# Kernel optimization log

Measured on AMD Instinct MI355X. Metric: run time of the kernel, lower is better.

The kernel has to match this reference:

```python
import jax, jax.numpy as jnp
import numpy as np

B, S, H, NH, HD = 2, 2048, 4096, 32, 128  # batch, seq, hidden, heads, head_dim
THETA = 10000.0
SCALE = HD ** -0.5


def setup_inputs() -> dict:
    key = jax.random.key(0)
    k1, k2, k3 = jax.random.split(key, 3)
    hidden_states = jax.random.normal(k1, (B, S, H), jnp.float32) * 0.02
    w_pack = jax.random.normal(k2, (3 * H, H), jnp.float32) * 0.02  # fused QKV weight
    w_o = jax.random.normal(k3, (H, H), jnp.float32) * 0.02
    positions = jnp.broadcast_to(jnp.arange(S, dtype=jnp.int32), (B, S))
    return {"positions": positions, "hidden_states": hidden_states,
            "w_pack": w_pack, "w_o": w_o}


def _apply_rope(x, positions):
    # x: [B, S, NH, HD]; neox-style (rotate-half) RoPE over full head_dim
    inv_freq = 1.0 / (THETA ** (jnp.arange(0, HD, 2, dtype=jnp.float32) / HD))  # [HD/2]
    ang = positions.astype(jnp.float32)[..., None] * inv_freq  # [B, S, HD/2]
    cos = jnp.cos(ang)[:, :, None, :]  # [B, S, 1, HD/2]
    sin = jnp.sin(ang)[:, :, None, :]
    x1, x2 = x[..., : HD // 2], x[..., HD // 2 :]
    return jnp.concatenate([x1 * cos - x2 * sin, x2 * cos + x1 * sin], axis=-1)


def reference(positions, hidden_states, w_pack, w_o):
    # Fused QKV projection then split (W_pack, bias-free)
    qkv = jnp.einsum('bsh,oh->bso', hidden_states, w_pack)  # [B, S, 3H]
    q, k, v = jnp.split(qkv, 3, axis=-1)
    q = q.reshape(B, S, NH, HD)
    k = k.reshape(B, S, NH, HD)
    v = v.reshape(B, S, NH, HD)
    q = _apply_rope(q, positions)
    k = _apply_rope(k, positions)
    # Causal scaled-dot-product attention
    scores = jnp.einsum('bqhd,bkhd->bhqk', q, k) * SCALE
    causal = jnp.tril(jnp.ones((S, S), dtype=bool))
    scores = jnp.where(causal, scores, jnp.float32(-1e9))
    probs = jax.nn.softmax(scores, axis=-1)
    attn = jnp.einsum('bhqk,bkhd->bqhd', probs, v).reshape(B, S, H)
    return jnp.einsum('bsh,oh->bso', attn, w_o)  # o_proj, bias-free
```

## Files before the change

### kernel.cpp

```cpp
#include <hip/hip_runtime.h>

typedef short short8 __attribute__((ext_vector_type(8)));
typedef float f32x4 __attribute__((ext_vector_type(4)));
typedef unsigned short u16;

static constexpr int BATCH = 2, S = 2048, H = 4096, NHEAD = 32, HDIM = 128;

__device__ __forceinline__ u16 f2b(float f) {
  union { float f; unsigned u; } v; v.f = f;
  return (u16)((v.u + 0x7fffu + ((v.u >> 16) & 1u)) >> 16);
}
__device__ __forceinline__ float b2f(u16 h) {
  union { unsigned u; float f; } v; v.u = ((unsigned)h) << 16;
  return v.f;
}

__device__ __forceinline__ void gl16(const u16* g, u16* l) {
  __builtin_amdgcn_global_load_lds((__attribute__((address_space(1))) void*)g,
                                   (__attribute__((address_space(3))) void*)l,
                                   16, 0, 0);
}

#define MFMA(acc, a, b) \
  acc = __builtin_amdgcn_mfma_f32_16x16x32_bf16(a, b, acc, 0, 0, 0)

__global__ __launch_bounds__(256) void cvt_bf16(const float* __restrict__ in,
                                                u16* __restrict__ out) {
  size_t i = ((size_t)blockIdx.x * 256 + threadIdx.x) * 4;
  float4 v = *(const float4*)(in + i);
  ushort4 o = { f2b(v.x), f2b(v.y), f2b(v.z), f2b(v.w) };
  *(ushort4*)(out + i) = o;
}

__global__ __launch_bounds__(256) void rope_table(float* __restrict__ tab) {
  int idx = blockIdx.x * 256 + threadIdx.x;
  int p = idx >> 6, f = idx & 63;
  float freq = __powf(10000.0f, -(float)f * (1.0f / 64.0f));
  float a = (float)p * freq;
  tab[(size_t)p * 128 + f] = cosf(a);
  tab[(size_t)p * 128 + 64 + f] = sinf(a);
}

template <int MODE>
__global__ __launch_bounds__(512, 2) void gemm256(
    const u16* __restrict__ A, const u16* __restrict__ B, void* __restrict__ C,
    int M, int N, int K, const int* __restrict__ pos,
    const float* __restrict__ tab, u16* __restrict__ qr, u16* __restrict__ kr,
    u16* __restrict__ vt) {
  __shared__ u16 SMEM[69632];
  u16* AL = SMEM;
  u16* BL = SMEM + 32768;
  const int nbn = N >> 8;
  const int nwg = (M >> 8) * nbn;
  const int bid = blockIdx.x;
  const int wg = (bid & 7) * (nwg >> 3) + (bid >> 3);
  const int bm = wg / nbn, bn = wg % nbn;
  const int tid = threadIdx.x, lane = tid & 63;
  const int w = tid >> 6, wm = w >> 2, wn = w & 3;
  const int hi = lane >> 4, lo = lane & 15;
  const int nk = K >> 6;

  const u16* Abase = A + (size_t)(bm * 256) * K;
  const u16* Bbase = B + (size_t)(bn * 256) * K;

#define STG_A(buf, half, kt)                                                   \
  { _Pragma("unroll") for (int i = 0; i < 2; ++i) {                            \
      int c = tid + i * 512, r = c >> 3, s = c & 7;                            \
      gl16(Abase + (size_t)((half) * 128 + r) * K + (kt) * 64 +                \
               ((s ^ (r & 7)) * 8),                                            \
           &AL[((buf) * 2 + (half)) * 8192 + c * 8]);                          \
    } }
#define STG_B(buf, half, kt)                                                   \
  { _Pragma("unroll") for (int i = 0; i < 2; ++i) {                            \
      int c = tid + i * 512, r = c >> 3, s = c & 7;                            \
      gl16(Bbase + (size_t)((half) * 128 + r) * K + (kt) * 64 +                \
               ((s ^ (r & 7)) * 8),                                            \
           &BL[((buf) * 2 + (half)) * 8192 + c * 8]);                          \
    } }
#define BARTOP()                                                               \
  do { __builtin_amdgcn_s_barrier();                                           \
       __builtin_amdgcn_sched_barrier(0); } while (0)

  f32x4 acc[8][4] = {};

  STG_A(0, 0, 0) STG_A(0, 1, 0) STG_B(0, 0, 0) STG_B(0, 1, 0)
  if (nk > 1) {
    STG_B(1, 0, 1) STG_B(1, 1, 1)
    asm volatile("s_waitcnt vmcnt(4)" ::: "memory");
  } else {
    asm volatile("s_waitcnt vmcnt(0)" ::: "memory");
  }
  __builtin_amdgcn_sched_barrier(0);

  short8 af[4][2], bfA[2][2], bfB[2][2];

  for (int t = 0; t < nk; ++t) {
    const int cur = t & 1;
    const u16* Awave = AL + (cur * 2 + wm) * 8192;
    const u16* Bwave = BL + (cur * 2 + (wn >> 1)) * 8192;
    const int lrB = (wn & 1) * 64;

    BARTOP();
    if (t + 1 < nk) STG_A(cur ^ 1, 0, t + 1)
#pragma unroll
    for (int mi = 0; mi < 4; ++mi)
#pragma unroll
      for (int ks = 0; ks < 2; ++ks)
        af[mi][ks] = *(const short8*)&Awave[(mi * 16 + lo) * 64 +
                                            (((ks * 4 + hi) ^ (lo & 7)) * 8)];
#pragma unroll
    for (int ni = 0; ni < 2; ++ni)
#pragma unroll
      for (int ks = 0; ks < 2; ++ks)
        bfA[ni][ks] = *(const short8*)&Bwave[(lrB + ni * 16 + lo) * 64 +
                                             (((ks * 4 + hi) ^ (lo & 7)) * 8)];

    BARTOP();
    if (t + 1 < nk) STG_A(cur ^ 1, 1, t + 1)
#pragma unroll
    for (int ni = 0; ni < 2; ++ni)
#pragma unroll
      for (int ks = 0; ks < 2; ++ks)
        bfB[ni][ks] = *(const short8*)&Bwave[(lrB + 32 + ni * 16 + lo) * 64 +
                                             (((ks * 4 + hi) ^ (lo & 7)) * 8)];
    __builtin_amdgcn_s_setprio(1);
#pragma unroll
    for (int mi = 0; mi < 4; ++mi)
#pragma unroll
      for (int ni = 0; ni < 2; ++ni)
#pragma unroll
        for (int ks = 0; ks < 2; ++ks)
          MFMA(acc[mi][ni], af[mi][ks], bfA[ni][ks]);
    __builtin_amdgcn_s_setprio(0);

    BARTOP();
    if (t + 2 < nk) STG_B(cur, 0, t + 2)
    __builtin_amdgcn_s_setprio(1);
#pragma unroll
    for (int mi = 0; mi < 4; ++mi)
#pragma unroll
      for (int ni = 0; ni < 2; ++ni)
#pragma unroll
        for (int ks = 0; ks < 2; ++ks)
          MFMA(acc[mi][2 + ni], af[mi][ks], bfB[ni][ks]);
    __builtin_amdgcn_s_setprio(0);
#pragma unroll
    for (int mi = 0; mi < 4; ++mi)
#pragma unroll
      for (int ks = 0; ks < 2; ++ks)
        af[mi][ks] = *(const short8*)&Awave[((64 + mi * 16 + lo)) * 64 +
                                            (((ks * 4 + hi) ^ (lo & 7)) * 8)];

    BARTOP();
    if (t + 2 < nk) STG_B(cur, 1, t + 2)
    __builtin_amdgcn_s_setprio(1);
#pragma unroll
    for (int mi = 0; mi < 4; ++mi)
#pragma unroll
      for (int ni = 0; ni < 2; ++ni)
#pragma unroll
        for (int ks = 0; ks < 2; ++ks)
          MFMA(acc[4 + mi][2 + ni], af[mi][ks], bfB[ni][ks]);
#pragma unroll
    for (int mi = 0; mi < 4; ++mi)
#pragma unroll
      for (int ni = 0; ni < 2; ++ni)
#pragma unroll
        for (int ks = 0; ks < 2; ++ks)
          MFMA(acc[4 + mi][ni], af[mi][ks], bfA[ni][ks]);
    __builtin_amdgcn_s_setprio(0);
    if (t + 2 < nk) {
      asm volatile("s_waitcnt vmcnt(4)" ::: "memory");
    } else {
      asm volatile("s_waitcnt vmcnt(0)" ::: "memory");
    }
    __builtin_amdgcn_sched_barrier(0);
  }

  if constexpr (MODE == 1) {
#pragma unroll
    for (int mf = 0; mf < 8; ++mf)
#pragma unroll
      for (int nf = 0; nf < 4; ++nf)
#pragma unroll
        for (int j = 0; j < 4; ++j) {
          size_t idx = (size_t)(bm * 256 + wm * 128 + mf * 16 + hi * 4 + j) * N +
                       bn * 256 + wn * 64 + nf * 16 + lo;
          ((float*)C)[idx] = acc[mf][nf][j];
        }
  } else {
    const int SP = 272;
    u16* E = SMEM;
    __syncthreads();
#pragma unroll
    for (int mf = 0; mf < 8; ++mf)
#pragma unroll
      for (int nf = 0; nf < 4; ++nf)
#pragma unroll
        for (int j = 0; j < 4; ++j)
          E[(wm * 128 + mf * 16 + hi * 4 + j) * SP + wn * 64 + nf * 16 + lo] =
              f2b(acc[mf][nf][j]);
    __syncthreads();

    const int grow0 = bm * 256, gcol0 = bn * 256;
    const int bb = grow0 >> 11, s0 = grow0 & 2047;
    if (gcol0 < 8192) {
      for (int task = tid; task < 8192; task += 512) {
        int row = task >> 5, g = task & 31;
        int gcol = gcol0 + g * 8;
        int d = gcol & 127, f0 = d & 63;
        int p = pos[grow0 + row];
        const float* cp = tab + (size_t)p * 128 + f0;
        float4 ca = *(const float4*)cp, cb = *(const float4*)(cp + 4);
        float4 sa = *(const float4*)(cp + 64), sb = *(const float4*)(cp + 68);
        float cv[8] = {ca.x, ca.y, ca.z, ca.w, cb.x, cb.y, cb.z, cb.w};
        float sv[8] = {sa.x, sa.y, sa.z, sa.w, sb.x, sb.y, sb.z, sb.w};
        short8 x = *(const short8*)&E[row * SP + g * 8];
        short8 xo = *(const short8*)&E[row * SP + (g ^ 8) * 8];
        float sgn = (d < 64) ? -1.0f : 1.0f;
        unsigned word[4];
#pragma unroll
        for (int pr = 0; pr < 4; ++pr) {
          float v0 = b2f((u16)x[2 * pr]) * cv[2 * pr] +
                     sgn * b2f((u16)xo[2 * pr]) * sv[2 * pr];
          float v1 = b2f((u16)x[2 * pr + 1]) * cv[2 * pr + 1] +
                     sgn * b2f((u16)xo[2 * pr + 1]) * sv[2 * pr + 1];
          word[pr] = (unsigned)f2b(v0) | ((unsigned)f2b(v1) << 16);
        }
        int hidx = gcol >> 7;
        u16* outp = (hidx < 32) ? qr : kr;
        int nh = (hidx < 32) ? hidx : hidx - 32;
        size_t dst = ((size_t)(bb * 32 + nh) * 2048 + (s0 + row)) * 128 + d;
        uint4 o = {word[0], word[1], word[2], word[3]};
        *(uint4*)&outp[dst] = o;
      }
    } else {
      for (int task = tid; task < 8192; task += 512) {
        int kbl = task >> 11;
        int hh = (task >> 10) & 1;
        int c = task & 1023;
        int f = c >> 6, l = c & 63;
        int ks2 = f >> 3, db = f & 7, hi2 = l >> 4, lo2 = l & 15;
        int base = (kbl * 64 + ks2 * 32 + hi2 * 8) * SP + hh * 128 + db * 16 + lo2;
        unsigned e0 = E[base], e1 = E[base + SP], e2 = E[base + 2 * SP],
                 e3 = E[base + 3 * SP], e4 = E[base + 4 * SP],
                 e5 = E[base + 5 * SP], e6 = E[base + 6 * SP],
                 e7 = E[base + 7 * SP];
        int nh = ((gcol0 - 8192) >> 7) + hh;
        size_t dst = ((size_t)(bb * 32 + nh) * 2048 + (s0 + kbl * 64)) * 128 +
                     (size_t)c * 8;
        uint4 o = {e0 | (e1 << 16), e2 | (e3 << 16), e4 | (e5 << 16),
                   e6 | (e7 << 16)};
        *(uint4*)&vt[dst] = o;
      }
    }
  }
}

__global__ __launch_bounds__(256, 2) void flash_fwd(const u16* __restrict__ q,
                                                    const u16* __restrict__ k,
                                                    const u16* __restrict__ vt,
                                                    u16* __restrict__ o) {
  __shared__ u16 KB[2][64 * 128];
  __shared__ u16 VB[2][64 * 128];
  __shared__ u16 Ps[4][16 * 64];
  const int nqt = S / 64;
  const int qt = (nqt - 1) - ((int)blockIdx.x % nqt);
  const int bh = blockIdx.x / nqt;
  const int tid = threadIdx.x, lane = tid & 63, w = tid >> 6;
  const int hi = lane >> 4, lo = lane & 15;

  const u16* qg = q + ((size_t)bh * S + qt * 64 + w * 16) * HDIM;
  short8 qf[4];
#pragma unroll
  for (int ks = 0; ks < 4; ++ks) {
    short8 r = *(const short8*)(qg + (size_t)lo * HDIM + ks * 32 + hi * 8);
    union { short8 s; u16 u[8]; } t; t.s = r;
#pragma unroll
    for (int e = 0; e < 8; ++e)
      t.u[e] = f2b(b2f(t.u[e]) * 0.08838834764831845f);
    qf[ks] = t.s;
  }

  float m_i[4], l_i[4];
  f32x4 oacc[8] = {};
#pragma unroll
  for (int j = 0; j < 4; ++j) { m_i[j] = -1e30f; l_i[j] = 0.0f; }

  const u16* kg = k + (size_t)bh * S * HDIM;
  const u16* vg = vt + (size_t)bh * S * HDIM;

#define STAGE(buf, kvbase)                                                  \
  {                                                                         \
    _Pragma("unroll") for (int i = 0; i < 4; ++i) {                         \
      int idx = i * 256 + tid, r = idx >> 4, gd = idx & 15;                 \
      gl16(kg + (size_t)((kvbase) + r) * HDIM + ((gd ^ (r & 7)) * 8),       \
           &KB[buf][idx * 8]);                                              \
    }                                                                       \
    _Pragma("unroll") for (int i = 0; i < 4; ++i) {                         \
      int idx = i * 256 + tid;                                              \
      gl16(vg + (size_t)(kvbase) * HDIM + idx * 8, &VB[buf][idx * 8]);      \
    }                                                                       \
  }

  STAGE(0, 0)
  int cur = 0;
  u16* PsW = &Ps[w][0];

  for (int kvt = 0; kvt <= qt; ++kvt) {
    if (kvt < qt) {
      STAGE(cur ^ 1, (kvt + 1) * 64)
      asm volatile("s_waitcnt vmcnt(8)" ::: "memory");
    } else {
      asm volatile("s_waitcnt vmcnt(0)" ::: "memory");
    }
    __builtin_amdgcn_s_barrier();
    __builtin_amdgcn_sched_barrier(0);
    const u16* Kc = &KB[cur][0];
    const u16* Vc = &VB[cur][0];

    f32x4 sc[4] = {};
#pragma unroll
    for (int ks = 0; ks < 4; ++ks) {
      const int colu = ks * 32 + hi * 8;
#pragma unroll
      for (int cb = 0; cb < 4; ++cb) {
        const int row = cb * 16 + lo;
        short8 kf = *(const short8*)&Kc[row * 128 + (colu ^ ((row & 7) << 3))];
        MFMA(sc[cb], qf[ks], kf);
      }
    }

    const int qrow = qt * 64 + w * 16 + hi * 4;
    const bool diag = (kvt == qt);
#pragma unroll
    for (int cb = 0; cb < 4; ++cb) {
      const int kvc = kvt * 64 + cb * 16 + lo;
#pragma unroll
      for (int j = 0; j < 4; ++j) {
        float sv = sc[cb][j];
        if (diag && kvc > qrow + j) sv = -1e30f;
        sc[cb][j] = sv;
      }
    }
    float rmax[4], rs[4];
#pragma unroll
    for (int j = 0; j < 4; ++j) {
      rmax[j] = fmaxf(fmaxf(sc[0][j], sc[1][j]), fmaxf(sc[2][j], sc[3][j]));
      for (int d = 8; d; d >>= 1) rmax[j] = fmaxf(rmax[j], __shfl_xor(rmax[j], d));
      float mn = fmaxf(m_i[j], rmax[j]);
      float sf = __expf(m_i[j] - mn);
      m_i[j] = mn; l_i[j] *= sf;
#pragma unroll
      for (int db = 0; db < 8; ++db) oacc[db][j] *= sf;
      rs[j] = 0.0f;
    }
#pragma unroll
    for (int cb = 0; cb < 4; ++cb)
#pragma unroll
      for (int j = 0; j < 4; ++j) {
        float p = __expf(sc[cb][j] - m_i[j]);
        sc[cb][j] = p; rs[j] += p;
      }
#pragma unroll
    for (int j = 0; j < 4; ++j) {
      for (int d = 8; d; d >>= 1) rs[j] += __shfl_xor(rs[j], d);
      l_i[j] += rs[j];
    }

#pragma unroll
    for (int cb = 0; cb < 4; ++cb)
#pragma unroll
      for (int j = 0; j < 4; ++j) {
        const int p = hi * 4 + j;
        PsW[p * 64 + ((cb * 16 + lo) ^ ((p & 7) << 3))] = f2b(sc[cb][j]);
      }
    short8 pf0 = *(const short8*)&PsW[lo * 64 + ((hi * 8) ^ ((lo & 7) << 3))];
    short8 pf1 = *(const short8*)&PsW[lo * 64 + ((32 + hi * 8) ^ ((lo & 7) << 3))];

#pragma unroll
    for (int ks2 = 0; ks2 < 2; ++ks2) {
      const short8 pf = ks2 ? pf1 : pf0;
#pragma unroll
      for (int db = 0; db < 8; ++db) {
        short8 vf = *(const short8*)&Vc[((ks2 * 8 + db) * 64 + lane) * 8];
        MFMA(oacc[db], pf, vf);
      }
    }
    __builtin_amdgcn_s_barrier();
    cur ^= 1;
  }

#pragma unroll
  for (int j = 0; j < 4; ++j) {
    float inv = 1.0f / l_i[j];
    int srow = qt * 64 + w * 16 + hi * 4 + j;
    const int b = bh >> 5, nh = bh & 31;
    size_t base = ((size_t)b * S + srow) * H + (size_t)nh * HDIM + lo;
#pragma unroll
    for (int db = 0; db < 8; ++db)
      o[base + db * 16] = f2b(oacc[db][j] * inv);
  }
}

extern "C" void kernel_launch(void* const* d_in, const int* in_sizes, int n_in,
                              void* d_out, int out_size, void* d_ws, size_t ws_size,
                              hipStream_t stream) {
  const int* pos = (const int*)d_in[0];
  const float* hs = (const float*)d_in[1];
  const float* wpack = (const float*)d_in[2];
  const float* wo = (const float*)d_in[3];
  float* out = (float*)d_out;
  char* ws = (char*)d_ws;
  u16* hs_b    = (u16*)(ws + 0UL);
  u16* wpack_b = (u16*)(ws + 33554432UL);
  u16* wo_b    = (u16*)(ws + 134217728UL);
  u16* v_t     = (u16*)(ws + 167772160UL);
  float* tab   = (float*)(ws + 201326592UL);
  u16* q_r     = (u16*)(ws + 268435456UL);
  u16* k_r     = (u16*)(ws + 301989888UL);
  u16* attn_b  = (u16*)(ws + 335544320UL);

  cvt_bf16<<<16384, 256, 0, stream>>>(hs, hs_b);
  cvt_bf16<<<49152, 256, 0, stream>>>(wpack, wpack_b);
  cvt_bf16<<<16384, 256, 0, stream>>>(wo, wo_b);
  rope_table<<<512, 256, 0, stream>>>(tab);
  gemm256<0><<<768, 512, 0, stream>>>(hs_b, wpack_b, nullptr, 4096, 12288, 4096,
                                      pos, tab, q_r, k_r, v_t);
  flash_fwd<<<64 * 32, 256, 0, stream>>>(q_r, k_r, v_t, attn_b);
  gemm256<1><<<256, 512, 0, stream>>>(attn_b, wo_b, out, 4096, 4096, 4096,
                                      nullptr, nullptr, nullptr, nullptr, nullptr);
}
```

Measured before the change: 855.9 us.

## Merge prep kernels into one launch and defer softmax row-sum reduction

Folds the three fp32-to-bf16 conversion launches and the RoPE table launch into a single prep kernel that dispatches on block index, removing three kernel launch gaps. In the flash attention loop, the per-tile cross-lane shuffle reduction of the softmax row sum is dropped: each lane keeps a partial sum and the reduction happens once before normalization. This is valid because the rescale factor is uniform across lanes. The causal mask is also placed under a diagonal-only branch, so off-diagonal tiles skip the comparisons.

```diff
diff --git a/kernel.cpp b/kernel.cpp
--- a/kernel.cpp
+++ b/kernel.cpp
@@ -24,21 +24,31 @@
 #define MFMA(acc, a, b) \
   acc = __builtin_amdgcn_mfma_f32_16x16x32_bf16(a, b, acc, 0, 0, 0)
 
-__global__ __launch_bounds__(256) void cvt_bf16(const float* __restrict__ in,
-                                                u16* __restrict__ out) {
-  size_t i = ((size_t)blockIdx.x * 256 + threadIdx.x) * 4;
-  float4 v = *(const float4*)(in + i);
-  ushort4 o = { f2b(v.x), f2b(v.y), f2b(v.z), f2b(v.w) };
-  *(ushort4*)(out + i) = o;
-}
-
-__global__ __launch_bounds__(256) void rope_table(float* __restrict__ tab) {
-  int idx = blockIdx.x * 256 + threadIdx.x;
-  int p = idx >> 6, f = idx & 63;
-  float freq = __powf(10000.0f, -(float)f * (1.0f / 64.0f));
-  float a = (float)p * freq;
-  tab[(size_t)p * 128 + f] = cosf(a);
-  tab[(size_t)p * 128 + 64 + f] = sinf(a);
+__global__ __launch_bounds__(256) void prep(const float* __restrict__ hs,
+                                            const float* __restrict__ wpack,
+                                            const float* __restrict__ wo,
+                                            u16* __restrict__ hs_b,
+                                            u16* __restrict__ wpack_b,
+                                            u16* __restrict__ wo_b,
+                                            float* __restrict__ tab) {
+  int b = blockIdx.x;
+  if (b < 81920) {
+    const float* in; u16* out; size_t off;
+    if (b < 16384)      { in = hs;    out = hs_b;    off = (size_t)b * 1024; }
+    else if (b < 65536) { in = wpack; out = wpack_b; off = (size_t)(b - 16384) * 1024; }
+    else                { in = wo;    out = wo_b;    off = (size_t)(b - 65536) * 1024; }
+    size_t i = off + threadIdx.x * 4;
+    float4 v = *(const float4*)(in + i);
+    ushort4 o = { f2b(v.x), f2b(v.y), f2b(v.z), f2b(v.w) };
+    *(ushort4*)(out + i) = o;
+  } else {
+    int idx = (b - 81920) * 256 + threadIdx.x;
+    int p = idx >> 6, f = idx & 63;
+    float freq = __powf(10000.0f, -(float)f * (1.0f / 64.0f));
+    float a = (float)p * freq;
+    tab[(size_t)p * 128 + f] = cosf(a);
+    tab[(size_t)p * 128 + 64 + f] = sinf(a);
+  }
 }
 
 template <int MODE>
@@ -282,10 +292,10 @@
     qf[ks] = t.s;
   }
 
-  float m_i[4], l_i[4];
+  float m_i[4], lsum[4];
   f32x4 oacc[8] = {};
 #pragma unroll
-  for (int j = 0; j < 4; ++j) { m_i[j] = -1e30f; l_i[j] = 0.0f; }
+  for (int j = 0; j < 4; ++j) { m_i[j] = -1e30f; lsum[j] = 0.0f; }
 
   const u16* kg = k + (size_t)bh * S * HDIM;
   const u16* vg = vt + (size_t)bh * S * HDIM;
@@ -331,42 +341,34 @@
       }
     }
 
-    const int qrow = qt * 64 + w * 16 + hi * 4;
-    const bool diag = (kvt == qt);
-#pragma unroll
-    for (int cb = 0; cb < 4; ++cb) {
-      const int kvc = kvt * 64 + cb * 16 + lo;
-#pragma unroll
-      for (int j = 0; j < 4; ++j) {
-        float sv = sc[cb][j];
-        if (diag && kvc > qrow + j) sv = -1e30f;
-        sc[cb][j] = sv;
-      }
-    }
-    float rmax[4], rs[4];
+    if (kvt == qt) {
+      const int qrow = qt * 64 + w * 16 + hi * 4;
+#pragma unroll
+      for (int cb = 0; cb < 4; ++cb) {
+        const int kvc = kvt * 64 + cb * 16 + lo;
+#pragma unroll
+        for (int j = 0; j < 4; ++j)
+          if (kvc > qrow + j) sc[cb][j] = -1e30f;
+      }
+    }
+    float rmax[4];
 #pragma unroll
     for (int j = 0; j < 4; ++j) {
       rmax[j] = fmaxf(fmaxf(sc[0][j], sc[1][j]), fmaxf(sc[2][j], sc[3][j]));
       for (int d = 8; d; d >>= 1) rmax[j] = fmaxf(rmax[j], __shfl_xor(rmax[j], d));
       float mn = fmaxf(m_i[j], rmax[j]);
       float sf = __expf(m_i[j] - mn);
-      m_i[j] = mn; l_i[j] *= sf;
+      m_i[j] = mn; lsum[j] *= sf;
 #pragma unroll
       for (int db = 0; db < 8; ++db) oacc[db][j] *= sf;
-      rs[j] = 0.0f;
     }
 #pragma unroll
     for (int cb = 0; cb < 4; ++cb)
 #pragma unroll
       for (int j = 0; j < 4; ++j) {
         float p = __expf(sc[cb][j] - m_i[j]);
-        sc[cb][j] = p; rs[j] += p;
-      }
-#pragma unroll
-    for (int j = 0; j < 4; ++j) {
-      for (int d = 8; d; d >>= 1) rs[j] += __shfl_xor(rs[j], d);
-      l_i[j] += rs[j];
-    }
+        sc[cb][j] = p; lsum[j] += p;
+      }
 
 #pragma unroll
     for (int cb = 0; cb < 4; ++cb)
@@ -393,7 +395,9 @@
 
 #pragma unroll
   for (int j = 0; j < 4; ++j) {
-    float inv = 1.0f / l_i[j];
+    float l = lsum[j];
+    for (int d = 8; d; d >>= 1) l += __shfl_xor(l, d);
+    float inv = 1.0f / l;
     int srow = qt * 64 + w * 16 + hi * 4 + j;
     const int b = bh >> 5, nh = bh & 31;
     size_t base = ((size_t)b * S + srow) * H + (size_t)nh * HDIM + lo;
@@ -421,10 +425,7 @@
   u16* k_r     = (u16*)(ws + 301989888UL);
   u16* attn_b  = (u16*)(ws + 335544320UL);
 
-  cvt_bf16<<<16384, 256, 0, stream>>>(hs, hs_b);
-  cvt_bf16<<<49152, 256, 0, stream>>>(wpack, wpack_b);
-  cvt_bf16<<<16384, 256, 0, stream>>>(wo, wo_b);
-  rope_table<<<512, 256, 0, stream>>>(tab);
+  prep<<<82432, 256, 0, stream>>>(hs, wpack, wo, hs_b, wpack_b, wo_b, tab);
   gemm256<0><<<768, 512, 0, stream>>>(hs_b, wpack_b, nullptr, 4096, 12288, 4096,
                                       pos, tab, q_r, k_r, v_t);
   flash_fwd<<<64 * 32, 256, 0, stream>>>(q_r, k_r, v_t, attn_b);
```

New measurement: 814.6 us. 1.05x faster.
